# Kernel tuning notes

Measured on AMD Instinct MI355X. Metric: run time of the kernel, lower is better.

The kernel has to match this reference:

```python
import jax, jax.numpy as jnp
import numpy as np

NUM_ANCHORS = 400_000
NUM_GTS = 64
NUM_CLASSES = 1
TOPK = 10
ALPHA = 1.0
BETA = 6.0
IMG = 640.0


def setup_inputs() -> dict:
    key = jax.random.key(0)
    k1, k2, k3, k4, k5, k6 = jax.random.split(key, 6)
    # anchor points uniformly over the image plane
    anc_points = jax.random.uniform(k1, (NUM_ANCHORS, 2), jnp.float32, 0.0, IMG)
    # predicted boxes: centered near the anchor point, valid xyxy
    pd_wh = jax.random.uniform(k2, (NUM_ANCHORS, 2), jnp.float32, 8.0, 96.0)
    pd_bboxes = jnp.concatenate([anc_points - pd_wh * 0.5, anc_points + pd_wh * 0.5], axis=-1)
    # predicted class scores in [0, 1] (post-sigmoid)
    pd_scores = jax.random.uniform(k3, (NUM_ANCHORS, NUM_CLASSES), jnp.float32)
    # GT boxes: random centers / sizes, valid xyxy
    gt_c = jax.random.uniform(k4, (NUM_GTS, 2), jnp.float32, 64.0, IMG - 64.0)
    gt_wh = jax.random.uniform(k5, (NUM_GTS, 2), jnp.float32, 16.0, 128.0)
    gt_bboxes = jnp.concatenate([gt_c - gt_wh * 0.5, gt_c + gt_wh * 0.5], axis=-1)
    gt_labels = jax.random.randint(k6, (NUM_GTS,), 0, NUM_CLASSES, dtype=jnp.int32)
    return {
        "pd_scores": pd_scores,
        "pd_bboxes": pd_bboxes,
        "anc_points": anc_points,
        "gt_labels": gt_labels,
        "gt_bboxes": gt_bboxes,
    }


def _box_iou(b1, b2):
    # b1: [A,4] xyxy, b2: [G,4] xyxy -> [A,G] pairwise IoU (torchvision box_iou math)
    lt = jnp.maximum(b1[:, None, :2], b2[None, :, :2])  # [A,G,2]
    rb = jnp.minimum(b1[:, None, 2:], b2[None, :, 2:])  # [A,G,2]
    wh = jnp.clip(rb - lt, 0.0)
    inter = wh[..., 0] * wh[..., 1]                      # [A,G]
    area1 = (b1[:, 2] - b1[:, 0]) * (b1[:, 3] - b1[:, 1])
    area2 = (b2[:, 2] - b2[:, 0]) * (b2[:, 3] - b2[:, 1])
    return inter / (area1[:, None] + area2[None, :] - inter)


def reference(pd_scores, pd_bboxes, anc_points, gt_labels, gt_bboxes):
    A = anc_points.shape[0]
    G = gt_bboxes.shape[0]
    # is anchor point inside each GT box -> [A,G] bool
    x, y = anc_points[:, 0:1], anc_points[:, 1:2]
    is_in_gts = ((x >= gt_bboxes[None, :, 0]) & (x <= gt_bboxes[None, :, 2]) &
                 (y >= gt_bboxes[None, :, 1]) & (y <= gt_bboxes[None, :, 3]))
    # Original gathers candidate anchors (inside >=1 GT) then computes metrics.
    # Equivalent dense form: non-candidates have is_in_gts row all-False so their
    # alignment metric is 0 for every GT and they are filtered by metric>0 below.
    iou = _box_iou(pd_bboxes, gt_bboxes)                         # [A,G]
    cls_scores = pd_scores[:, gt_labels]                          # [A,G]
    cls_scores = cls_scores * is_in_gts.astype(cls_scores.dtype)
    metric = (cls_scores ** ALPHA) * (iou ** BETA)                # [A,G]
    # per-GT top-k anchors by alignment metric
    _, topk_idx = jax.lax.top_k(metric.T, TOPK)                   # [G,k]
    topk_mask = jnp.zeros((A, G), dtype=bool)
    topk_mask = topk_mask.at[topk_idx.T, jnp.arange(G)[None, :]].set(True)
    topk_mask = topk_mask & (metric > 0)
    is_assigned = topk_mask.any(axis=1)                           # [A]
    best_gt = jnp.argmax(metric, axis=1)                          # [A]
    fg_mask = is_assigned
    assigned_gt_idx = jnp.where(fg_mask, best_gt, 0).astype(jnp.int32)
    return fg_mask, assigned_gt_idx
```

## Files before the change

### kernel.cpp

```cpp
#include <hip/hip_runtime.h>

#define NUM_A    400000
#define NUM_G    64
#define TOPK     10
#define CHUNKS   64
#define CHUNK_SZ (NUM_A / CHUNKS)
#define GGROUP   4
#define NGROUPS  (NUM_G / GGROUP)
#define CAP      768
#define SENT_I   0x7fffffff

__device__ __forceinline__ bool better(float m1, int a1, float m2, int a2) {
    return (m1 > m2) || ((m1 == m2) && (a1 < a2));
}

__device__ __forceinline__ float iou_metric(
    float px1, float py1, float px2, float py2, float parea, float score,
    float gx1, float gy1, float gx2, float gy2, float garea)
{
    float ltx = fmaxf(px1, gx1);
    float lty = fmaxf(py1, gy1);
    float rbx = fminf(px2, gx2);
    float rby = fminf(py2, gy2);
    float w = fmaxf(rbx - ltx, 0.0f);
    float h = fmaxf(rby - lty, 0.0f);
    float inter = w * h;
    float iou = inter / (parea + garea - inter);
    float iou2 = iou * iou;
    float iou6 = iou2 * iou2 * iou2;
    return score * iou6;
}

__device__ __forceinline__ void wave_max_pair(float& bv, int& bi) {
#pragma unroll
    for (int s = 1; s < 64; s <<= 1) {
        float ov = __shfl_xor(bv, s, 64);
        int   oi = __shfl_xor(bi, s, 64);
        if (better(ov, oi, bv, bi)) { bv = ov; bi = oi; }
    }
}

__global__ __launch_bounds__(256) void topk_partial_kernel(
    const float* __restrict__ pd_scores,
    const float* __restrict__ pd_bboxes,
    const float* __restrict__ anc_points,
    const float* __restrict__ gt_bboxes,
    float* __restrict__ pval,
    int*   __restrict__ pidx)
{
    const int c   = blockIdx.x;
    const int gg  = blockIdx.y;
    const int tid = threadIdx.x;
    const int g0  = gg * GGROUP;

    __shared__ int s_cnt[GGROUP];
    __shared__ int s_cand[GGROUP][CAP];

    if (tid < GGROUP) s_cnt[tid] = 0;

    float gx1[GGROUP], gy1[GGROUP], gx2[GGROUP], gy2[GGROUP];
#pragma unroll
    for (int j = 0; j < GGROUP; ++j) {
        float4 gb = ((const float4*)gt_bboxes)[g0 + j];
        gx1[j] = gb.x; gy1[j] = gb.y; gx2[j] = gb.z; gy2[j] = gb.w;
    }
    __syncthreads();

    const int p0 = c * (CHUNK_SZ / 2);
    const int p1 = p0 + CHUNK_SZ / 2;
    for (int p = p0 + tid; p < p1; p += 256) {
        float4 aq = ((const float4*)anc_points)[p];
        const int a2 = 2 * p;
#pragma unroll
        for (int j = 0; j < GGROUP; ++j) {
            bool in0 = (aq.x >= gx1[j]) && (aq.x <= gx2[j]) &&
                       (aq.y >= gy1[j]) && (aq.y <= gy2[j]);
            bool in1 = (aq.z >= gx1[j]) && (aq.z <= gx2[j]) &&
                       (aq.w >= gy1[j]) && (aq.w <= gy2[j]);
            if (in0) { int q = atomicAdd(&s_cnt[j], 1); if (q < CAP) s_cand[j][q] = a2; }
            if (in1) { int q = atomicAdd(&s_cnt[j], 1); if (q < CAP) s_cand[j][q] = a2 + 1; }
        }
    }
    __syncthreads();

    const int wj   = tid >> 6;
    const int lane = tid & 63;

    float4 gb = ((const float4*)gt_bboxes)[g0 + wj];
    const float garea = (gb.z - gb.x) * (gb.w - gb.y);
    const int n = min(s_cnt[wj], CAP);

    float tv[TOPK]; int ti[TOPK];
#pragma unroll
    for (int k = 0; k < TOPK; ++k) { tv[k] = 0.0f; ti[k] = SENT_I; }

    for (int i = lane; i < n; i += 64) {
        const int a = s_cand[wj][i];
        float4 pb = ((const float4*)pd_bboxes)[a];
        float sc = pd_scores[a];
        float parea = (pb.z - pb.x) * (pb.w - pb.y);
        float m = iou_metric(pb.x, pb.y, pb.z, pb.w, parea, sc,
                             gb.x, gb.y, gb.z, gb.w, garea);
        if (better(m, a, tv[TOPK - 1], ti[TOPK - 1])) {
#pragma unroll
            for (int k = TOPK - 1; k >= 1; --k) {
                bool gp = better(m, a, tv[k - 1], ti[k - 1]);
                bool gc = better(m, a, tv[k],     ti[k]);
                tv[k] = gp ? tv[k - 1] : (gc ? m : tv[k]);
                ti[k] = gp ? ti[k - 1] : (gc ? a : ti[k]);
            }
            if (better(m, a, tv[0], ti[0])) { tv[0] = m; ti[0] = a; }
        }
    }

    float outv = 0.0f; int outi = SENT_I;
#pragma unroll
    for (int k = 0; k < TOPK; ++k) {
        float bv = tv[0]; int bi = ti[0];
        wave_max_pair(bv, bi);
        bool win = (ti[0] == bi);
#pragma unroll
        for (int j = 0; j < TOPK - 1; ++j) {
            tv[j] = win ? tv[j + 1] : tv[j];
            ti[j] = win ? ti[j + 1] : ti[j];
        }
        if (win) { tv[TOPK - 1] = 0.0f; ti[TOPK - 1] = SENT_I; }
        if (lane == k) { outv = bv; outi = bi; }
    }
    if (lane < TOPK) {
        const int g = g0 + wj;
        pval[(g * CHUNKS + c) * TOPK + lane] = outv;
        pidx[(g * CHUNKS + c) * TOPK + lane] = outi;
    }
}

__global__ __launch_bounds__(64) void merge_assign_kernel(
    const float* __restrict__ pval,
    const int*   __restrict__ pidx,
    const float* __restrict__ pd_scores,
    const float* __restrict__ pd_bboxes,
    const float* __restrict__ anc_points,
    const float* __restrict__ gt_bboxes,
    int* __restrict__ out_fg,
    int* __restrict__ out_idx)
{
    const int g    = blockIdx.x;
    const int lane = threadIdx.x;

    float4 mygt = ((const float4*)gt_bboxes)[lane];
    float  myga = (mygt.z - mygt.x) * (mygt.w - mygt.y);

    float tv[TOPK]; int ti[TOPK];
    const float* pv = pval + (g * CHUNKS + lane) * TOPK;
    const int*   pi = pidx + (g * CHUNKS + lane) * TOPK;
#pragma unroll
    for (int k = 0; k < TOPK; ++k) { tv[k] = pv[k]; ti[k] = pi[k]; }

#pragma unroll
    for (int k = 0; k < TOPK; ++k) {
        float bv = tv[0]; int bi = ti[0];
        wave_max_pair(bv, bi);
        bool win = (ti[0] == bi);
#pragma unroll
        for (int j = 0; j < TOPK - 1; ++j) {
            tv[j] = win ? tv[j + 1] : tv[j];
            ti[j] = win ? ti[j + 1] : ti[j];
        }
        if (win) { tv[TOPK - 1] = 0.0f; ti[TOPK - 1] = SENT_I; }

        if (bv > 0.0f) {
            const int a = bi;
            float2 ap = ((const float2*)anc_points)[a];
            float4 pb = ((const float4*)pd_bboxes)[a];
            float  sc = pd_scores[a];
            float parea = (pb.z - pb.x) * (pb.w - pb.y);
            bool in = (ap.x >= mygt.x) && (ap.x <= mygt.z) &&
                      (ap.y >= mygt.y) && (ap.y <= mygt.w);
            float m = iou_metric(pb.x, pb.y, pb.z, pb.w, parea,
                                 in ? sc : 0.0f,
                                 mygt.x, mygt.y, mygt.z, mygt.w, myga);
            float av = m; int ag = lane;
#pragma unroll
            for (int s = 1; s < 64; s <<= 1) {
                float ov = __shfl_xor(av, s, 64);
                int   og = __shfl_xor(ag, s, 64);
                if ((ov > av) || ((ov == av) && (og < ag))) { av = ov; ag = og; }
            }
            if (lane == 0) { out_fg[a] = 1; out_idx[a] = ag; }
        }
    }
}

extern "C" void kernel_launch(void* const* d_in, const int* in_sizes, int n_in,
                              void* d_out, int out_size, void* d_ws, size_t ws_size,
                              hipStream_t stream) {
    const float* pd_scores  = (const float*)d_in[0];
    const float* pd_bboxes  = (const float*)d_in[1];
    const float* anc_points = (const float*)d_in[2];
    const float* gt_bboxes  = (const float*)d_in[4];

    const int npairs = NUM_G * CHUNKS * TOPK;
    float* pval = (float*)d_ws;
    int*   pidx = (int*)(pval + npairs);

    int* out_fg  = (int*)d_out;
    int* out_idx = out_fg + NUM_A;

    hipMemsetAsync(d_out, 0, 2 * NUM_A * sizeof(int), stream);

    dim3 g1(CHUNKS, NGROUPS);
    topk_partial_kernel<<<g1, 256, 0, stream>>>(
        pd_scores, pd_bboxes, anc_points, gt_bboxes, pval, pidx);
    merge_assign_kernel<<<NUM_G, 64, 0, stream>>>(
        pval, pidx, pd_scores, pd_bboxes, anc_points, gt_bboxes,
        out_fg, out_idx);
}
```

Before: 104.5 us.

## Fuse output zeroing into topk kernel, use wave-aggregated ballot appends, widen GT groups

Drops the separate hipMemsetAsync and instead has every thread of the topk_partial kernel zero one int4 of the output, saving a launch and a pass. Candidate appends now use a ballot, one leader atomicAdd and a popcount offset per wave, replacing per-lane LDS atomics. Each block now handles 8 GTs with 512 threads, so anchor points are read half as often. Lanes past the chunk end are masked with a valid flag. The larger block raises register and LDS pressure per block and halves the block count in the second phase's per-wave top-k work distribution.

```diff
diff --git a/kernel.cpp b/kernel.cpp
--- a/kernel.cpp
+++ b/kernel.cpp
@@ -5,8 +5,9 @@
 #define TOPK     10
 #define CHUNKS   64
 #define CHUNK_SZ (NUM_A / CHUNKS)
-#define GGROUP   4
+#define GGROUP   8
 #define NGROUPS  (NUM_G / GGROUP)
+#define BLK      512
 #define CAP      768
 #define SENT_I   0x7fffffff
 
@@ -40,19 +41,44 @@
     }
 }
 
-__global__ __launch_bounds__(256) void topk_partial_kernel(
+__device__ __forceinline__ void ballot_append(
+    bool in, int a, int* cnt, int* list, int lane)
+{
+    unsigned long long mask = __ballot(in);
+    if (mask) {
+        int leader = __ffsll((long long)mask) - 1;
+        int base = 0;
+        if (lane == leader) base = atomicAdd(cnt, __popcll(mask));
+        base = __shfl(base, leader, 64);
+        if (in) {
+            int off = __popcll(mask & ((1ull << lane) - 1ull));
+            int q = base + off;
+            if (q < CAP) list[q] = a;
+        }
+    }
+}
+
+__global__ __launch_bounds__(BLK) void topk_partial_kernel(
     const float* __restrict__ pd_scores,
     const float* __restrict__ pd_bboxes,
     const float* __restrict__ anc_points,
     const float* __restrict__ gt_bboxes,
     float* __restrict__ pval,
-    int*   __restrict__ pidx)
+    int*   __restrict__ pidx,
+    int*   __restrict__ out_zero)
 {
     const int c   = blockIdx.x;
     const int gg  = blockIdx.y;
     const int tid = threadIdx.x;
     const int g0  = gg * GGROUP;
 
+    {
+        const int bid = blockIdx.y * gridDim.x + blockIdx.x;
+        const int t   = bid * BLK + tid;
+        int4* o4 = (int4*)out_zero;
+        if (t < (2 * NUM_A) / 4) o4[t] = make_int4(0, 0, 0, 0);
+    }
+
     __shared__ int s_cnt[GGROUP];
     __shared__ int s_cand[GGROUP][CAP];
 
@@ -66,25 +92,32 @@
     }
     __syncthreads();
 
+    const int lane = tid & 63;
+
     const int p0 = c * (CHUNK_SZ / 2);
     const int p1 = p0 + CHUNK_SZ / 2;
-    for (int p = p0 + tid; p < p1; p += 256) {
-        float4 aq = ((const float4*)anc_points)[p];
-        const int a2 = 2 * p;
+    const int niter = (CHUNK_SZ / 2 + BLK - 1) / BLK;
+    for (int it = 0; it < niter; ++it) {
+        const int p = p0 + it * BLK + tid;
+        const bool valid = (p < p1);
+        const int pc = valid ? p : (p1 - 1);
+        float4 aq = ((const float4*)anc_points)[pc];
+        const int a2 = 2 * pc;
 #pragma unroll
         for (int j = 0; j < GGROUP; ++j) {
-            bool in0 = (aq.x >= gx1[j]) && (aq.x <= gx2[j]) &&
+            bool in0 = valid &&
+                       (aq.x >= gx1[j]) && (aq.x <= gx2[j]) &&
                        (aq.y >= gy1[j]) && (aq.y <= gy2[j]);
-            bool in1 = (aq.z >= gx1[j]) && (aq.z <= gx2[j]) &&
+            bool in1 = valid &&
+                       (aq.z >= gx1[j]) && (aq.z <= gx2[j]) &&
                        (aq.w >= gy1[j]) && (aq.w <= gy2[j]);
-            if (in0) { int q = atomicAdd(&s_cnt[j], 1); if (q < CAP) s_cand[j][q] = a2; }
-            if (in1) { int q = atomicAdd(&s_cnt[j], 1); if (q < CAP) s_cand[j][q] = a2 + 1; }
+            ballot_append(in0, a2,     &s_cnt[j], s_cand[j], lane);
+            ballot_append(in1, a2 + 1, &s_cnt[j], s_cand[j], lane);
         }
     }
     __syncthreads();
 
-    const int wj   = tid >> 6;
-    const int lane = tid & 63;
+    const int wj = tid >> 6;
 
     float4 gb = ((const float4*)gt_bboxes)[g0 + wj];
     const float garea = (gb.z - gb.x) * (gb.w - gb.y);
@@ -206,11 +239,10 @@
     int* out_fg  = (int*)d_out;
     int* out_idx = out_fg + NUM_A;
 
-    hipMemsetAsync(d_out, 0, 2 * NUM_A * sizeof(int), stream);
-
     dim3 g1(CHUNKS, NGROUPS);
-    topk_partial_kernel<<<g1, 256, 0, stream>>>(
-        pd_scores, pd_bboxes, anc_points, gt_bboxes, pval, pidx);
+    topk_partial_kernel<<<g1, BLK, 0, stream>>>(
+        pd_scores, pd_bboxes, anc_points, gt_bboxes, pval, pidx,
+        (int*)d_out);
     merge_assign_kernel<<<NUM_G, 64, 0, stream>>>(
         pval, pidx, pd_scores, pd_bboxes, anc_points, gt_bboxes,
         out_fg, out_idx);
```

After: 111.3 us. 1.07x slower.
